# Kernel tuning notes

Measured on AMD Instinct MI355X. Metric: run time of the kernel, lower is better.

Reference implementation:

```python
import jax, jax.numpy as jnp
import numpy as np

N_NODES = 50000
N_EDGES = 800000
IN_DIM = 64
OUT_DIM = 64
HID = OUT_DIM // 2  # 32
N_LAYERS = 9  # layer_num; layer_num >= 7 => no temporal conv, conv dropout unused


def _layernorm(x, w, b, eps=1e-5):
    mu = jnp.mean(x, axis=-1, keepdims=True)
    var = jnp.var(x, axis=-1, keepdims=True)
    return (x - mu) * jax.lax.rsqrt(var + eps) * w + b


def _conv(x, Wp, Wn, Ws, src, tgt, pos_m, neg_m):
    # relation-wise gather -> linear -> masked merge -> single scatter_add
    xs = x[src]  # [E, d_in]
    m = jnp.where(pos_m[:, None], xs @ Wp.T, 0.0) + jnp.where(neg_m[:, None], xs @ Wn.T, 0.0)
    agg = jax.ops.segment_sum(m, tgt, num_segments=N_NODES)
    return agg + x @ Ws.T


def _asfr(x, ln_w, ln_b, gw, gb):
    xn = _layernorm(x, ln_w, ln_b)
    w = jax.nn.sigmoid(xn @ gw.T + gb)
    w1 = jnp.where(w > 0.5, 1.0, w)
    w2 = jnp.where(w > 0.5, 0.0, w)
    x1 = w1 * x
    x2 = w2 * x
    h = x.shape[1] // 2
    return jnp.concatenate([x1[:, :h] + x2[:, h:], x1[:, h:] + x2[:, :h]], axis=1)


def setup_inputs() -> dict:
    key = jax.random.key(0)
    ks = jax.random.split(key, 24)
    init_emb = jax.random.normal(ks[0], (N_NODES, IN_DIM), dtype=jnp.float32)
    src = jax.random.randint(ks[1], (N_EDGES,), 0, N_NODES)
    tgt = jax.random.randint(ks[2], (N_EDGES,), 0, N_NODES)
    sign = jnp.where(jax.random.uniform(ks[3], (N_EDGES,)) > 0.5, 1, -1).astype(jnp.int64)
    edge_index_s = jnp.stack([src, tgt, sign], axis=1).astype(jnp.int64)

    def w(k, shape, fan_in):
        return jax.random.normal(k, shape, dtype=jnp.float32) * (1.0 / np.sqrt(fan_in))

    inp = dict(init_emb=init_emb, edge_index_s=edge_index_s)
    # conv1: in 64 -> 32, relations pos/neg + self loop (no bias)
    inp["W1_pos"] = w(ks[4], (HID, IN_DIM), IN_DIM)
    inp["W1_neg"] = w(ks[5], (HID, IN_DIM), IN_DIM)
    inp["W1_self"] = w(ks[6], (HID, IN_DIM), IN_DIM)
    # 8 further convs: 32 -> 32, stacked
    L = N_LAYERS - 1
    inp["Wl_pos"] = w(ks[7], (L, HID, HID), HID)
    inp["Wl_neg"] = w(ks[8], (L, HID, HID), HID)
    inp["Wl_self"] = w(ks[9], (L, HID, HID), HID)
    # ASFR
    inp["asfr_ln_w"] = jnp.ones((HID,), jnp.float32)
    inp["asfr_ln_b"] = jnp.zeros((HID,), jnp.float32)
    inp["asfr_gate_w"] = w(ks[10], (HID, HID), HID)
    inp["asfr_gate_b"] = jnp.zeros((HID,), jnp.float32)
    # projection 32 -> 64
    inp["proj_w"] = w(ks[11], (OUT_DIM, HID), HID)
    inp["proj_b"] = jnp.zeros((OUT_DIM,), jnp.float32)
    # readout MLP: 64 -> 64 -> 64 -> 1, layernorm + relu between
    inp["mlp_w1"] = w(ks[12], (OUT_DIM, OUT_DIM), OUT_DIM)
    inp["mlp_b1"] = jnp.zeros((OUT_DIM,), jnp.float32)
    inp["mlp_ln1_w"] = jnp.ones((OUT_DIM,), jnp.float32)
    inp["mlp_ln1_b"] = jnp.zeros((OUT_DIM,), jnp.float32)
    inp["mlp_w2"] = w(ks[13], (OUT_DIM, OUT_DIM), OUT_DIM)
    inp["mlp_b2"] = jnp.zeros((OUT_DIM,), jnp.float32)
    inp["mlp_ln2_w"] = jnp.ones((OUT_DIM,), jnp.float32)
    inp["mlp_ln2_b"] = jnp.zeros((OUT_DIM,), jnp.float32)
    inp["mlp_w3"] = w(ks[14], (1, OUT_DIM), OUT_DIM)
    inp["mlp_b3"] = jnp.zeros((1,), jnp.float32)
    return inp


def reference(init_emb, edge_index_s, W1_pos, W1_neg, W1_self, Wl_pos, Wl_neg, Wl_self,
              asfr_ln_w, asfr_ln_b, asfr_gate_w, asfr_gate_b, proj_w, proj_b,
              mlp_w1, mlp_b1, mlp_ln1_w, mlp_ln1_b, mlp_w2, mlp_b2,
              mlp_ln2_w, mlp_ln2_b, mlp_w3, mlp_b3):
    src = edge_index_s[:, 0]
    tgt = edge_index_s[:, 1]
    sign = edge_index_s[:, 2]
    pos_m = sign > 0
    neg_m = sign < 0

    z = jax.nn.elu(_conv(init_emb, W1_pos, W1_neg, W1_self, src, tgt, pos_m, neg_m))
    z = _asfr(z, asfr_ln_w, asfr_ln_b, asfr_gate_w, asfr_gate_b)
    for i in range(Wl_pos.shape[0]):
        z_new = jax.nn.elu(_conv(z, Wl_pos[i], Wl_neg[i], Wl_self[i], src, tgt, pos_m, neg_m))
        z = z_new if i == 0 else z_new + 0.1 * z
    z = jax.nn.elu(z @ proj_w.T + proj_b)
    # readout MLP (eval mode: dropout identity)
    h = jax.nn.relu(_layernorm(z @ mlp_w1.T + mlp_b1, mlp_ln1_w, mlp_ln1_b))
    h = jax.nn.relu(_layernorm(h @ mlp_w2.T + mlp_b2, mlp_ln2_w, mlp_ln2_b))
    prob = jax.nn.sigmoid(h @ mlp_w3.T + mlp_b3)
    return (z, prob)
```

## Files before the change

kernel.cpp:

```cpp
#include <hip/hip_runtime.h>
#include <hip/hip_bf16.h>

#define NODES 50000
#define EDGES 800000
#define BSH 8
#define NBUCK 196
#define NBIN_BLOCKS 391

__device__ __forceinline__ float elu1(float x) { return x > 0.f ? x : expm1f(x); }

union F4 { float4 v; float f[4]; };

__global__ __launch_bounds__(256) void k_hist2(const int* __restrict__ ei, int* __restrict__ deg,
                                               int* __restrict__ bucket_cnt) {
  __shared__ int cnt[NBUCK];
  int t = threadIdx.x;
  for (int i = t; i < NBUCK; i += 256) cnt[i] = 0;
  __syncthreads();
  int base = blockIdx.x * 2048;
#pragma unroll
  for (int i = 0; i < 8; i++) {
    int e = base + i * 256 + t;
    if (e < EDGES) {
      int tgt = ei[e * 3 + 1];
      atomicAdd(deg + tgt, 1);
      atomicAdd(&cnt[tgt >> BSH], 1);
    }
  }
  __syncthreads();
  for (int i = t; i < NBUCK; i += 256)
    if (cnt[i]) atomicAdd(bucket_cnt + i, cnt[i]);
}

__global__ __launch_bounds__(512) void k_scan1(const int* __restrict__ deg, int* __restrict__ offs,
                                               int* __restrict__ bsum) {
  __shared__ int s[512];
  int t = threadIdx.x, i = blockIdx.x * 512 + t;
  int v = (i < NODES) ? deg[i] : 0;
  s[t] = v;
  __syncthreads();
  for (int o = 1; o < 512; o <<= 1) {
    int x = (t >= o) ? s[t - o] : 0;
    __syncthreads();
    s[t] += x;
    __syncthreads();
  }
  if (i < NODES) offs[i] = s[t] - v;
  if (t == 511) bsum[blockIdx.x] = s[511];
}

__global__ __launch_bounds__(128) void k_scan2(int* __restrict__ bsum, int nb) {
  __shared__ int s[128];
  int t = threadIdx.x;
  int v = (t < nb) ? bsum[t] : 0;
  s[t] = v;
  __syncthreads();
  for (int o = 1; o < 128; o <<= 1) {
    int x = (t >= o) ? s[t - o] : 0;
    __syncthreads();
    s[t] += x;
    __syncthreads();
  }
  if (t < nb) bsum[t] = s[t] - v;
}

__global__ __launch_bounds__(512) void k_scan3(int* __restrict__ offs, const int* __restrict__ bsum) {
  int i = blockIdx.x * 512 + threadIdx.x;
  if (i < NODES) offs[i] += bsum[blockIdx.x];
  if (i == 0) offs[NODES] = EDGES;
}

__global__ __launch_bounds__(256) void k_bscan(const int* __restrict__ bucket_cnt,
                                               int* __restrict__ bucket_base,
                                               int* __restrict__ bucket_cursor) {
  __shared__ int s[256];
  int t = threadIdx.x;
  int v = (t < NBUCK) ? bucket_cnt[t] : 0;
  s[t] = v;
  __syncthreads();
  for (int o = 1; o < 256; o <<= 1) {
    int x = (t >= o) ? s[t - o] : 0;
    __syncthreads();
    s[t] += x;
    __syncthreads();
  }
  if (t < NBUCK) { int e = s[t] - v; bucket_base[t] = e; bucket_cursor[t] = e; }
}

__global__ __launch_bounds__(256) void k_bin(const int* __restrict__ ei,
                                             int* __restrict__ bucket_cursor,
                                             uint2* __restrict__ binned) {
  __shared__ int cnt[NBUCK], base[NBUCK];
  int t = threadIdx.x;
  for (int i = t; i < NBUCK; i += 256) cnt[i] = 0;
  __syncthreads();
  int eb = blockIdx.x * 2048;
#pragma unroll
  for (int i = 0; i < 8; i++) {
    int e = eb + i * 256 + t;
    if (e < EDGES) atomicAdd(&cnt[ei[e * 3 + 1] >> BSH], 1);
  }
  __syncthreads();
  for (int i = t; i < NBUCK; i += 256) {
    int c = cnt[i];
    base[i] = c ? atomicAdd(bucket_cursor + i, c) : 0;
    cnt[i] = 0;
  }
  __syncthreads();
#pragma unroll
  for (int i = 0; i < 8; i++) {
    int e = eb + i * 256 + t;
    if (e < EDGES) {
      int src = ei[e * 3 + 0];
      int tgt = ei[e * 3 + 1];
      int sg  = ei[e * 3 + 2];
      unsigned val = (unsigned)src | (sg < 0 ? 0x80000000u : 0u);
      int bkt = tgt >> BSH;
      int r = atomicAdd(&cnt[bkt], 1);
      binned[base[bkt] + r] = make_uint2(val, (unsigned)tgt);
    }
  }
}

__global__ __launch_bounds__(256) void k_scatter2(const uint2* __restrict__ binned,
                                                  const int* __restrict__ bucket_base,
                                                  const int* __restrict__ bucket_cnt,
                                                  const int* __restrict__ offs,
                                                  unsigned* __restrict__ perm) {
  __shared__ int cur[256];
  int b = blockIdx.x, t = threadIdx.x;
  int t0 = b << BSH;
  cur[t] = (t0 + t < NODES) ? offs[t0 + t] : 0;
  __syncthreads();
  int n = bucket_cnt[b], bb = bucket_base[b];
  for (int i = t; i < n; i += 256) {
    uint2 e = binned[bb + i];
    int p = atomicAdd(&cur[e.y - t0], 1);
    perm[p] = e.x;
  }
}

__global__ __launch_bounds__(256) void k_lin64(const float* __restrict__ x,
    const float* __restrict__ Wp, const float* __restrict__ Wn, const float* __restrict__ Ws,
    __hip_bfloat16* __restrict__ ypb, __hip_bfloat16* __restrict__ ynb, float* __restrict__ ys) {
  constexpr int K4 = 16;
  __shared__ float4 wp[K4][32], wn[K4][32], wsm[K4][32];
  __shared__ float4 xs[8][K4];
  for (int i = threadIdx.x; i < 32 * K4; i += 256) {
    int k4 = i >> 5, c = i & 31;
    wp[k4][c]  = ((const float4*)Wp)[c * K4 + k4];
    wn[k4][c]  = ((const float4*)Wn)[c * K4 + k4];
    wsm[k4][c] = ((const float4*)Ws)[c * K4 + k4];
  }
  int base = blockIdx.x * 8;
  for (int i = threadIdx.x; i < 8 * K4; i += 256) {
    int r = i / K4, k4 = i - r * K4;
    xs[r][k4] = ((const float4*)(x + (size_t)(base + r) * 64))[k4];
  }
  __syncthreads();
  int lane = threadIdx.x & 31, local = threadIdx.x >> 5;
  float ap = 0.f, an = 0.f, asf = 0.f;
#pragma unroll
  for (int k4 = 0; k4 < K4; k4++) {
    float4 xv = xs[local][k4];
    float4 a = wp[k4][lane], b = wn[k4][lane], c = wsm[k4][lane];
    ap  = fmaf(xv.w, a.w, fmaf(xv.z, a.z, fmaf(xv.y, a.y, fmaf(xv.x, a.x, ap))));
    an  = fmaf(xv.w, b.w, fmaf(xv.z, b.z, fmaf(xv.y, b.y, fmaf(xv.x, b.x, an))));
    asf = fmaf(xv.w, c.w, fmaf(xv.z, c.z, fmaf(xv.y, c.y, fmaf(xv.x, c.x, asf))));
  }
  size_t o = (size_t)(base + local) * 32 + lane;
  ypb[o] = __float2bfloat16(ap);
  ynb[o] = __float2bfloat16(an);
  ys[o] = asf;
}

#define ACC8(A, V)                                   \
  A[0] += __uint_as_float((V).x << 16);              \
  A[1] += __uint_as_float((V).x & 0xffff0000u);      \
  A[2] += __uint_as_float((V).y << 16);              \
  A[3] += __uint_as_float((V).y & 0xffff0000u);      \
  A[4] += __uint_as_float((V).z << 16);              \
  A[5] += __uint_as_float((V).z & 0xffff0000u);      \
  A[6] += __uint_as_float((V).w << 16);              \
  A[7] += __uint_as_float((V).w & 0xffff0000u);

template <int DO_ASFR, int DO_RES, int DO_LIN, int WRITE_Z>
__global__ __launch_bounds__(256) void k_layer(
    const unsigned short* __restrict__ ypi, const unsigned short* __restrict__ yni,
    float* __restrict__ ys,
    const unsigned* __restrict__ perm, const int* __restrict__ offs,
    float* __restrict__ z,
    const float* __restrict__ lnw, const float* __restrict__ lnb,
    const float* __restrict__ gw, const float* __restrict__ gb,
    const float* __restrict__ Wp, const float* __restrict__ Wn, const float* __restrict__ Ws,
    __hip_bfloat16* __restrict__ ypo, __hip_bfloat16* __restrict__ yno) {
  __shared__ float4 wps[8][32], wns[8][32], wss[8][32], gws[8][32];
  __shared__ float zrow[8][36], xrow[8][36];
  int t = threadIdx.x;
  if (DO_LIN) {
    int k4 = t >> 5, c = t & 31;
    wps[k4][c] = ((const float4*)Wp)[c * 8 + k4];
    wns[k4][c] = ((const float4*)Wn)[c * 8 + k4];
    wss[k4][c] = ((const float4*)Ws)[c * 8 + k4];
    if (DO_ASFR) gws[k4][c] = ((const float4*)gw)[c * 8 + k4];
  }
  int lane = t & 31, local = t >> 5;
  int node = blockIdx.x * 8 + local;
  int es = lane >> 2, fs = lane & 3;
  int beg = offs[node], end = offs[node + 1];
  float a0[8], a1[8], a2[8], a3[8];
#pragma unroll
  for (int i = 0; i < 8; i++) { a0[i] = 0.f; a1[i] = 0.f; a2[i] = 0.f; a3[i] = 0.f; }
  for (int base = beg; base < end; base += 32) {
    unsigned pe = (base + lane < end) ? perm[base + lane] : 0u;
    int rem = end - base;
    unsigned u0 = __shfl(pe, es, 32);
    unsigned u1 = __shfl(pe, es + 8, 32);
    const unsigned short* p0 = (u0 >> 31) ? yni : ypi;
    const unsigned short* p1 = (u1 >> 31) ? yni : ypi;
    uint4 v0 = *((const uint4*)(p0 + (size_t)(u0 & 0x7FFFFFFFu) * 32) + fs);
    uint4 v1 = *((const uint4*)(p1 + (size_t)(u1 & 0x7FFFFFFFu) * 32) + fs);
    if (es < rem) { ACC8(a0, v0); }
    if (es + 8 < rem) { ACC8(a1, v1); }
    if (rem > 16) {
      unsigned u2 = __shfl(pe, es + 16, 32);
      unsigned u3 = __shfl(pe, es + 24, 32);
      const unsigned short* p2 = (u2 >> 31) ? yni : ypi;
      const unsigned short* p3 = (u3 >> 31) ? yni : ypi;
      uint4 v2 = *((const uint4*)(p2 + (size_t)(u2 & 0x7FFFFFFFu) * 32) + fs);
      uint4 v3 = *((const uint4*)(p3 + (size_t)(u3 & 0x7FFFFFFFu) * 32) + fs);
      if (es + 16 < rem) { ACC8(a2, v2); }
      if (es + 24 < rem) { ACC8(a3, v3); }
    }
  }
#pragma unroll
  for (int i = 0; i < 8; i++) a0[i] += (a1[i] + a2[i]) + a3[i];
#pragma unroll
  for (int m = 4; m <= 16; m <<= 1) {
#pragma unroll
    for (int i = 0; i < 8; i++) a0[i] += __shfl_xor(a0[i], m, 32);
  }
  if (es == 0) {
    const float* ysr = ys + (size_t)node * 32 + fs * 8;
    F4 s0, s1;
    s0.v = *(const float4*)ysr;
    s1.v = *(const float4*)(ysr + 4);
    float o[8];
#pragma unroll
    for (int i = 0; i < 4; i++) o[i] = elu1(a0[i] + s0.f[i]);
#pragma unroll
    for (int i = 0; i < 4; i++) o[4 + i] = elu1(a0[4 + i] + s1.f[i]);
    if (DO_RES) {
      const float* rr = z + (size_t)node * 32 + fs * 8;
      F4 r0, r1;
      r0.v = *(const float4*)rr;
      r1.v = *(const float4*)(rr + 4);
#pragma unroll
      for (int i = 0; i < 4; i++) { o[i] += 0.1f * r0.f[i]; o[4 + i] += 0.1f * r1.f[i]; }
    }
#pragma unroll
    for (int i = 0; i < 8; i++) zrow[local][fs * 8 + i] = o[i];
    if (WRITE_Z) {
      float* zw = z + (size_t)node * 32 + fs * 8;
      *(float4*)zw = make_float4(o[0], o[1], o[2], o[3]);
      *(float4*)(zw + 4) = make_float4(o[4], o[5], o[6], o[7]);
    }
  }
  __syncthreads();
  if (!DO_LIN) return;
  if (DO_ASFR) {
    float v = zrow[local][lane];
    float s = v;
#pragma unroll
    for (int m = 16; m; m >>= 1) s += __shfl_xor(s, m, 32);
    float mu = s * (1.f / 32.f);
    float d = v - mu, sq = d * d;
#pragma unroll
    for (int m = 16; m; m >>= 1) sq += __shfl_xor(sq, m, 32);
    float xn = d * rsqrtf(sq * (1.f / 32.f) + 1e-5f) * lnw[lane] + lnb[lane];
    xrow[local][lane] = xn;
    float ga = gb[lane];
#pragma unroll
    for (int k4 = 0; k4 < 8; k4++) {
      float4 xv = *((const float4*)&xrow[local][0] + k4);
      float4 w = gws[k4][lane];
      ga = fmaf(xv.w, w.w, fmaf(xv.z, w.z, fmaf(xv.y, w.y, fmaf(xv.x, w.x, ga))));
    }
    float g = 1.f / (1.f + __expf(-ga));
    float w1 = g > 0.5f ? 1.f : g;
    float w2 = g > 0.5f ? 0.f : g;
    float zn = w1 * v + __shfl_xor(w2 * v, 16, 32);
    zrow[local][lane] = zn;
  }
  float ap = 0.f, an = 0.f, asf = 0.f;
#pragma unroll
  for (int k4 = 0; k4 < 8; k4++) {
    float4 xv = *((const float4*)&zrow[local][0] + k4);
    float4 a2w = wps[k4][lane], b2 = wns[k4][lane], c2 = wss[k4][lane];
    ap  = fmaf(xv.w, a2w.w, fmaf(xv.z, a2w.z, fmaf(xv.y, a2w.y, fmaf(xv.x, a2w.x, ap))));
    an  = fmaf(xv.w, b2.w, fmaf(xv.z, b2.z, fmaf(xv.y, b2.y, fmaf(xv.x, b2.x, an))));
    asf = fmaf(xv.w, c2.w, fmaf(xv.z, c2.z, fmaf(xv.y, c2.y, fmaf(xv.x, c2.x, asf))));
  }
  size_t o = (size_t)node * 32 + lane;
  ypo[o] = __float2bfloat16(ap);
  yno[o] = __float2bfloat16(an);
  ys[o] = asf;
}

__global__ __launch_bounds__(256) void k_mlp(const float* __restrict__ z,
    const float* __restrict__ pw, const float* __restrict__ pb,
    const float* __restrict__ w1, const float* __restrict__ b1,
    const float* __restrict__ l1w, const float* __restrict__ l1b,
    const float* __restrict__ w2, const float* __restrict__ b2,
    const float* __restrict__ l2w, const float* __restrict__ l2b,
    const float* __restrict__ w3, const float* __restrict__ b3,
    float* __restrict__ outz, float* __restrict__ outp) {
  __shared__ float4 wbuf[1536];
  __shared__ float4 hbuf4[32 * 17];
  __shared__ float pb_s[64], b1_s[64], l1w_s[64], l1b_s[64], b2_s[64], l2w_s[64], l2b_s[64], w3_s[64];
  int t = threadIdx.x;
  for (int i = t; i < 512; i += 256) {
    int k = i >> 4, j4 = i & 15;
    float4 v;
    v.x = pw[(j4 * 4 + 0) * 32 + k]; v.y = pw[(j4 * 4 + 1) * 32 + k];
    v.z = pw[(j4 * 4 + 2) * 32 + k]; v.w = pw[(j4 * 4 + 3) * 32 + k];
    wbuf[i] = v;
  }
  for (int i = t; i < 1024; i += 256) {
    int k = i >> 4, j4 = i & 15;
    float4 v;
    v.x = w1[(j4 * 4 + 0) * 64 + k]; v.y = w1[(j4 * 4 + 1) * 64 + k];
    v.z = w1[(j4 * 4 + 2) * 64 + k]; v.w = w1[(j4 * 4 + 3) * 64 + k];
    wbuf[512 + i] = v;
  }
  if (t < 64) {
    pb_s[t] = pb[t]; b1_s[t] = b1[t]; l1w_s[t] = l1w[t]; l1b_s[t] = l1b[t];
    b2_s[t] = b2[t]; l2w_s[t] = l2w[t]; l2b_s[t] = l2b[t]; w3_s[t] = w3[t];
  }
  __syncthreads();
  int g = t >> 3, q = t & 7;
  int node = blockIdx.x * 32 + g;
  bool live = node < NODES;
  float bb3 = b3[0];
  float acc[8], h[8];
  if (live) {
    hbuf4[g * 17 + q] = ((const float4*)(z + (size_t)node * 32))[q];
#pragma unroll
    for (int i = 0; i < 8; i++) acc[i] = pb_s[q * 8 + i];
#pragma unroll 2
    for (int k4 = 0; k4 < 8; k4++) {
      F4 hv; hv.v = hbuf4[g * 17 + k4];
#pragma unroll
      for (int c = 0; c < 4; c++) {
        float hk = hv.f[c];
        float4 wa = wbuf[(k4 * 4 + c) * 16 + q * 2];
        float4 wb = wbuf[(k4 * 4 + c) * 16 + q * 2 + 1];
        acc[0] = fmaf(hk, wa.x, acc[0]); acc[1] = fmaf(hk, wa.y, acc[1]);
        acc[2] = fmaf(hk, wa.z, acc[2]); acc[3] = fmaf(hk, wa.w, acc[3]);
        acc[4] = fmaf(hk, wb.x, acc[4]); acc[5] = fmaf(hk, wb.y, acc[5]);
        acc[6] = fmaf(hk, wb.z, acc[6]); acc[7] = fmaf(hk, wb.w, acc[7]);
      }
    }
#pragma unroll
    for (int i = 0; i < 8; i++) h[i] = elu1(acc[i]);
    float4 h0 = make_float4(h[0], h[1], h[2], h[3]);
    float4 h1 = make_float4(h[4], h[5], h[6], h[7]);
    float4* oz = (float4*)(outz + (size_t)node * 64 + q * 8);
    oz[0] = h0; oz[1] = h1;
    hbuf4[g * 17 + 2 * q] = h0;
    hbuf4[g * 17 + 2 * q + 1] = h1;
#pragma unroll
    for (int i = 0; i < 8; i++) acc[i] = b1_s[q * 8 + i];
#pragma unroll 2
    for (int k4 = 0; k4 < 16; k4++) {
      F4 hv; hv.v = hbuf4[g * 17 + k4];
#pragma unroll
      for (int c = 0; c < 4; c++) {
        float hk = hv.f[c];
        float4 wa = wbuf[512 + (k4 * 4 + c) * 16 + q * 2];
        float4 wb = wbuf[512 + (k4 * 4 + c) * 16 + q * 2 + 1];
        acc[0] = fmaf(hk, wa.x, acc[0]); acc[1] = fmaf(hk, wa.y, acc[1]);
        acc[2] = fmaf(hk, wa.z, acc[2]); acc[3] = fmaf(hk, wa.w, acc[3]);
        acc[4] = fmaf(hk, wb.x, acc[4]); acc[5] = fmaf(hk, wb.y, acc[5]);
        acc[6] = fmaf(hk, wb.z, acc[6]); acc[7] = fmaf(hk, wb.w, acc[7]);
      }
    }
  }
  __syncthreads();
  for (int i = t; i < 1024; i += 256) {
    int k = i >> 4, j4 = i & 15;
    float4 v;
    v.x = w2[(j4 * 4 + 0) * 64 + k]; v.y = w2[(j4 * 4 + 1) * 64 + k];
    v.z = w2[(j4 * 4 + 2) * 64 + k]; v.w = w2[(j4 * 4 + 3) * 64 + k];
    wbuf[i] = v;
  }
  if (live) {
    float s = 0.f;
#pragma unroll
    for (int i = 0; i < 8; i++) s += acc[i];
    s += __shfl_xor(s, 1, 8); s += __shfl_xor(s, 2, 8); s += __shfl_xor(s, 4, 8);
    float mu = s * (1.f / 64.f);
    float vs = 0.f;
#pragma unroll
    for (int i = 0; i < 8; i++) { float dd = acc[i] - mu; vs += dd * dd; }
    vs += __shfl_xor(vs, 1, 8); vs += __shfl_xor(vs, 2, 8); vs += __shfl_xor(vs, 4, 8);
    float rs = rsqrtf(vs * (1.f / 64.f) + 1e-5f);
#pragma unroll
    for (int i = 0; i < 8; i++)
      h[i] = fmaxf((acc[i] - mu) * rs * l1w_s[q * 8 + i] + l1b_s[q * 8 + i], 0.f);
  }
  __syncthreads();
  if (!live) return;
  hbuf4[g * 17 + 2 * q] = make_float4(h[0], h[1], h[2], h[3]);
  hbuf4[g * 17 + 2 * q + 1] = make_float4(h[4], h[5], h[6], h[7]);
#pragma unroll
  for (int i = 0; i < 8; i++) acc[i] = b2_s[q * 8 + i];
#pragma unroll 2
  for (int k4 = 0; k4 < 16; k4++) {
    F4 hv; hv.v = hbuf4[g * 17 + k4];
#pragma unroll
    for (int c = 0; c < 4; c++) {
      float hk = hv.f[c];
      float4 wa = wbuf[(k4 * 4 + c) * 16 + q * 2];
      float4 wb = wbuf[(k4 * 4 + c) * 16 + q * 2 + 1];
      acc[0] = fmaf(hk, wa.x, acc[0]); acc[1] = fmaf(hk, wa.y, acc[1]);
      acc[2] = fmaf(hk, wa.z, acc[2]); acc[3] = fmaf(hk, wa.w, acc[3]);
      acc[4] = fmaf(hk, wb.x, acc[4]); acc[5] = fmaf(hk, wb.y, acc[5]);
      acc[6] = fmaf(hk, wb.z, acc[6]); acc[7] = fmaf(hk, wb.w, acc[7]);
    }
  }
  {
    float s = 0.f;
#pragma unroll
    for (int i = 0; i < 8; i++) s += acc[i];
    s += __shfl_xor(s, 1, 8); s += __shfl_xor(s, 2, 8); s += __shfl_xor(s, 4, 8);
    float mu = s * (1.f / 64.f);
    float vs = 0.f;
#pragma unroll
    for (int i = 0; i < 8; i++) { float dd = acc[i] - mu; vs += dd * dd; }
    vs += __shfl_xor(vs, 1, 8); vs += __shfl_xor(vs, 2, 8); vs += __shfl_xor(vs, 4, 8);
    float rs = rsqrtf(vs * (1.f / 64.f) + 1e-5f);
    float p = 0.f;
#pragma unroll
    for (int i = 0; i < 8; i++) {
      float hv2 = fmaxf((acc[i] - mu) * rs * l2w_s[q * 8 + i] + l2b_s[q * 8 + i], 0.f);
      p = fmaf(hv2, w3_s[q * 8 + i], p);
    }
    p += __shfl_xor(p, 1, 8); p += __shfl_xor(p, 2, 8); p += __shfl_xor(p, 4, 8);
    if (q == 0) outp[node] = 1.f / (1.f + __expf(-(p + bb3)));
  }
}

extern "C" void kernel_launch(void* const* d_in, const int* in_sizes, int n_in,
                              void* d_out, int out_size, void* d_ws, size_t ws_size,
                              hipStream_t stream) {
  const float* init_emb = (const float*)d_in[0];
  const int*   ei  = (const int*)d_in[1];
  const float* W1p = (const float*)d_in[2];
  const float* W1n = (const float*)d_in[3];
  const float* W1s = (const float*)d_in[4];
  const float* Wlp = (const float*)d_in[5];
  const float* Wln = (const float*)d_in[6];
  const float* Wls = (const float*)d_in[7];
  const float* lnw = (const float*)d_in[8];
  const float* lnb = (const float*)d_in[9];
  const float* gw  = (const float*)d_in[10];
  const float* gb  = (const float*)d_in[11];
  const float* pw  = (const float*)d_in[12];
  const float* pb  = (const float*)d_in[13];
  const float* w1  = (const float*)d_in[14];
  const float* b1  = (const float*)d_in[15];
  const float* l1w = (const float*)d_in[16];
  const float* l1b = (const float*)d_in[17];
  const float* w2  = (const float*)d_in[18];
  const float* b2  = (const float*)d_in[19];
  const float* l2w = (const float*)d_in[20];
  const float* l2b = (const float*)d_in[21];
  const float* w3  = (const float*)d_in[22];
  const float* b3  = (const float*)d_in[23];

  char* ws = (char*)d_ws;
  size_t off = 0;
  auto alloc = [&](size_t b) { void* p = ws + off; off = (off + b + 255) & ~(size_t)255; return p; };
  __hip_bfloat16* ypA = (__hip_bfloat16*)alloc(NODES * 32 * 2);
  __hip_bfloat16* ynA = (__hip_bfloat16*)alloc(NODES * 32 * 2);
  __hip_bfloat16* ypB = (__hip_bfloat16*)alloc(NODES * 32 * 2);
  __hip_bfloat16* ynB = (__hip_bfloat16*)alloc(NODES * 32 * 2);
  float*    ysel   = (float*)alloc(NODES * 32 * 4);
  float*    zbuf   = (float*)alloc(NODES * 32 * 4);
  unsigned* perm   = (unsigned*)alloc(EDGES * 4);
  int*      deg    = (int*)alloc(NODES * 4);
  int*      offs   = (int*)alloc((NODES + 1) * 4);
  int*      bsum   = (int*)alloc(128 * 4);
  int*      bucket_cnt    = (int*)alloc(NBUCK * 4);
  int*      bucket_base   = (int*)alloc(NBUCK * 4);
  int*      bucket_cursor = (int*)alloc(NBUCK * 4);
  uint2*    binned = (uint2*)ypA;

  hipMemsetAsync(deg, 0, NODES * 4, stream);
  hipMemsetAsync(bucket_cnt, 0, NBUCK * 4, stream);
  k_hist2<<<NBIN_BLOCKS, 256, 0, stream>>>(ei, deg, bucket_cnt);
  int nb = (NODES + 511) / 512;
  k_scan1<<<nb, 512, 0, stream>>>(deg, offs, bsum);
  k_scan2<<<1, 128, 0, stream>>>(bsum, nb);
  k_scan3<<<nb, 512, 0, stream>>>(offs, bsum);
  k_bscan<<<1, 256, 0, stream>>>(bucket_cnt, bucket_base, bucket_cursor);
  k_bin<<<NBIN_BLOCKS, 256, 0, stream>>>(ei, bucket_cursor, binned);
  k_scatter2<<<NBUCK, 256, 0, stream>>>(binned, bucket_base, bucket_cnt, offs, perm);

  const int G = NODES / 8;
  k_lin64<<<G, 256, 0, stream>>>(init_emb, W1p, W1n, W1s, ypA, ynA, ysel);
  k_layer<1, 0, 1, 0><<<G, 256, 0, stream>>>((const unsigned short*)ypA, (const unsigned short*)ynA,
      ysel, perm, offs, zbuf, lnw, lnb, gw, gb, Wlp, Wln, Wls, ypB, ynB);
  k_layer<0, 0, 1, 1><<<G, 256, 0, stream>>>((const unsigned short*)ypB, (const unsigned short*)ynB,
      ysel, perm, offs, zbuf, nullptr, nullptr, nullptr, nullptr,
      Wlp + 1024, Wln + 1024, Wls + 1024, ypA, ynA);
  const __hip_bfloat16* yin_p = ypA; const __hip_bfloat16* yin_n = ynA;
  __hip_bfloat16* yout_p = ypB; __hip_bfloat16* yout_n = ynB;
  for (int i = 1; i < 7; i++) {
    k_layer<0, 1, 1, 1><<<G, 256, 0, stream>>>((const unsigned short*)yin_p, (const unsigned short*)yin_n,
        ysel, perm, offs, zbuf, nullptr, nullptr, nullptr, nullptr,
        Wlp + (i + 1) * 1024, Wln + (i + 1) * 1024, Wls + (i + 1) * 1024, yout_p, yout_n);
    const __hip_bfloat16* tp = yin_p; const __hip_bfloat16* tn = yin_n;
    yin_p = yout_p; yin_n = yout_n;
    yout_p = (__hip_bfloat16*)tp; yout_n = (__hip_bfloat16*)tn;
  }
  k_layer<0, 1, 0, 1><<<G, 256, 0, stream>>>((const unsigned short*)yin_p, (const unsigned short*)yin_n,
      ysel, perm, offs, zbuf, nullptr, nullptr, nullptr, nullptr,
      nullptr, nullptr, nullptr, nullptr, nullptr);

  float* outz = (float*)d_out;
  float* outp = outz + (size_t)NODES * 64;
  k_mlp<<<(NODES + 31) / 32, 256, 0, stream>>>(zbuf, pw, pb, w1, b1, l1w, l1b,
                                               w2, b2, l2w, l2b, w3, b3, outz, outp);
}
```

Before: 395.0 us.

## Pack binned edges into 32-bit words and process four nodes per MLP thread group

The binning pass now packs the source index, the sign bit and the target's low 8 bits into one 32-bit word instead of a uint2, halving the binned edge traffic. The scatter pass unpacks it and rebuilds the original sign-in-top-bit format. The readout MLP kernel now handles 128 nodes per block, four per 8-lane group, so each shared-memory weight load is reused across four nodes. The price is more registers per thread and fewer blocks, and the packing assumes node ids fit in 16 bits (NODES is 50000, so they do).

```diff
diff --git a/kernel.cpp b/kernel.cpp
--- a/kernel.cpp
+++ b/kernel.cpp
@@ -89,7 +89,7 @@
 
 __global__ __launch_bounds__(256) void k_bin(const int* __restrict__ ei,
                                              int* __restrict__ bucket_cursor,
-                                             uint2* __restrict__ binned) {
+                                             unsigned* __restrict__ binned) {
   __shared__ int cnt[NBUCK], base[NBUCK];
   int t = threadIdx.x;
   for (int i = t; i < NBUCK; i += 256) cnt[i] = 0;
@@ -114,15 +114,15 @@
       int src = ei[e * 3 + 0];
       int tgt = ei[e * 3 + 1];
       int sg  = ei[e * 3 + 2];
-      unsigned val = (unsigned)src | (sg < 0 ? 0x80000000u : 0u);
+      unsigned val = (unsigned)src | (sg < 0 ? 0x10000u : 0u) | ((unsigned)(tgt & 255) << 17);
       int bkt = tgt >> BSH;
       int r = atomicAdd(&cnt[bkt], 1);
-      binned[base[bkt] + r] = make_uint2(val, (unsigned)tgt);
-    }
-  }
-}
-
-__global__ __launch_bounds__(256) void k_scatter2(const uint2* __restrict__ binned,
+      binned[base[bkt] + r] = val;
+    }
+  }
+}
+
+__global__ __launch_bounds__(256) void k_scatter2(const unsigned* __restrict__ binned,
                                                   const int* __restrict__ bucket_base,
                                                   const int* __restrict__ bucket_cnt,
                                                   const int* __restrict__ offs,
@@ -134,9 +134,9 @@
   __syncthreads();
   int n = bucket_cnt[b], bb = bucket_base[b];
   for (int i = t; i < n; i += 256) {
-    uint2 e = binned[bb + i];
-    int p = atomicAdd(&cur[e.y - t0], 1);
-    perm[p] = e.x;
+    unsigned e = binned[bb + i];
+    int p = atomicAdd(&cur[(e >> 17) & 255], 1);
+    perm[p] = (e & 0xFFFFu) | ((e & 0x10000u) << 15);
   }
 }
 
@@ -316,7 +316,7 @@
     const float* __restrict__ w3, const float* __restrict__ b3,
     float* __restrict__ outz, float* __restrict__ outp) {
   __shared__ float4 wbuf[1536];
-  __shared__ float4 hbuf4[32 * 17];
+  __shared__ float4 hbuf4[128 * 17];
   __shared__ float pb_s[64], b1_s[64], l1w_s[64], l1b_s[64], b2_s[64], l2w_s[64], l2b_s[64], w3_s[64];
   int t = threadIdx.x;
   for (int i = t; i < 512; i += 256) {
@@ -339,50 +339,72 @@
   }
   __syncthreads();
   int g = t >> 3, q = t & 7;
-  int node = blockIdx.x * 32 + g;
-  bool live = node < NODES;
+  int nb0 = blockIdx.x * 128 + g;
   float bb3 = b3[0];
-  float acc[8], h[8];
-  if (live) {
-    hbuf4[g * 17 + q] = ((const float4*)(z + (size_t)node * 32))[q];
-#pragma unroll
-    for (int i = 0; i < 8; i++) acc[i] = pb_s[q * 8 + i];
+  bool live[4];
+#pragma unroll
+  for (int n = 0; n < 4; n++) live[n] = (nb0 + 32 * n) < NODES;
+  float acc[4][8], h[4][8];
+#pragma unroll
+  for (int n = 0; n < 4; n++)
+    if (live[n])
+      hbuf4[(n * 32 + g) * 17 + q] = ((const float4*)(z + (size_t)(nb0 + 32 * n) * 32))[q];
+#pragma unroll
+  for (int n = 0; n < 4; n++)
+#pragma unroll
+    for (int i = 0; i < 8; i++) acc[n][i] = pb_s[q * 8 + i];
 #pragma unroll 2
-    for (int k4 = 0; k4 < 8; k4++) {
-      F4 hv; hv.v = hbuf4[g * 17 + k4];
-#pragma unroll
-      for (int c = 0; c < 4; c++) {
-        float hk = hv.f[c];
-        float4 wa = wbuf[(k4 * 4 + c) * 16 + q * 2];
-        float4 wb = wbuf[(k4 * 4 + c) * 16 + q * 2 + 1];
-        acc[0] = fmaf(hk, wa.x, acc[0]); acc[1] = fmaf(hk, wa.y, acc[1]);
-        acc[2] = fmaf(hk, wa.z, acc[2]); acc[3] = fmaf(hk, wa.w, acc[3]);
-        acc[4] = fmaf(hk, wb.x, acc[4]); acc[5] = fmaf(hk, wb.y, acc[5]);
-        acc[6] = fmaf(hk, wb.z, acc[6]); acc[7] = fmaf(hk, wb.w, acc[7]);
+  for (int k4 = 0; k4 < 8; k4++) {
+    F4 hv[4];
+#pragma unroll
+    for (int n = 0; n < 4; n++) hv[n].v = hbuf4[(n * 32 + g) * 17 + k4];
+#pragma unroll
+    for (int c = 0; c < 4; c++) {
+      float4 wa = wbuf[(k4 * 4 + c) * 16 + q * 2];
+      float4 wb = wbuf[(k4 * 4 + c) * 16 + q * 2 + 1];
+#pragma unroll
+      for (int n = 0; n < 4; n++) {
+        float hk = hv[n].f[c];
+        acc[n][0] = fmaf(hk, wa.x, acc[n][0]); acc[n][1] = fmaf(hk, wa.y, acc[n][1]);
+        acc[n][2] = fmaf(hk, wa.z, acc[n][2]); acc[n][3] = fmaf(hk, wa.w, acc[n][3]);
+        acc[n][4] = fmaf(hk, wb.x, acc[n][4]); acc[n][5] = fmaf(hk, wb.y, acc[n][5]);
+        acc[n][6] = fmaf(hk, wb.z, acc[n][6]); acc[n][7] = fmaf(hk, wb.w, acc[n][7]);
       }
     }
-#pragma unroll
-    for (int i = 0; i < 8; i++) h[i] = elu1(acc[i]);
-    float4 h0 = make_float4(h[0], h[1], h[2], h[3]);
-    float4 h1 = make_float4(h[4], h[5], h[6], h[7]);
-    float4* oz = (float4*)(outz + (size_t)node * 64 + q * 8);
-    oz[0] = h0; oz[1] = h1;
-    hbuf4[g * 17 + 2 * q] = h0;
-    hbuf4[g * 17 + 2 * q + 1] = h1;
-#pragma unroll
-    for (int i = 0; i < 8; i++) acc[i] = b1_s[q * 8 + i];
+  }
+#pragma unroll
+  for (int n = 0; n < 4; n++) {
+#pragma unroll
+    for (int i = 0; i < 8; i++) h[n][i] = elu1(acc[n][i]);
+    float4 h0 = make_float4(h[n][0], h[n][1], h[n][2], h[n][3]);
+    float4 h1 = make_float4(h[n][4], h[n][5], h[n][6], h[n][7]);
+    if (live[n]) {
+      float4* oz = (float4*)(outz + (size_t)(nb0 + 32 * n) * 64 + q * 8);
+      oz[0] = h0; oz[1] = h1;
+    }
+    hbuf4[(n * 32 + g) * 17 + 2 * q] = h0;
+    hbuf4[(n * 32 + g) * 17 + 2 * q + 1] = h1;
+  }
+#pragma unroll
+  for (int n = 0; n < 4; n++)
+#pragma unroll
+    for (int i = 0; i < 8; i++) acc[n][i] = b1_s[q * 8 + i];
 #pragma unroll 2
-    for (int k4 = 0; k4 < 16; k4++) {
-      F4 hv; hv.v = hbuf4[g * 17 + k4];
-#pragma unroll
-      for (int c = 0; c < 4; c++) {
-        float hk = hv.f[c];
-        float4 wa = wbuf[512 + (k4 * 4 + c) * 16 + q * 2];
-        float4 wb = wbuf[512 + (k4 * 4 + c) * 16 + q * 2 + 1];
-        acc[0] = fmaf(hk, wa.x, acc[0]); acc[1] = fmaf(hk, wa.y, acc[1]);
-        acc[2] = fmaf(hk, wa.z, acc[2]); acc[3] = fmaf(hk, wa.w, acc[3]);
-        acc[4] = fmaf(hk, wb.x, acc[4]); acc[5] = fmaf(hk, wb.y, acc[5]);
-        acc[6] = fmaf(hk, wb.z, acc[6]); acc[7] = fmaf(hk, wb.w, acc[7]);
+  for (int k4 = 0; k4 < 16; k4++) {
+    F4 hv[4];
+#pragma unroll
+    for (int n = 0; n < 4; n++) hv[n].v = hbuf4[(n * 32 + g) * 17 + k4];
+#pragma unroll
+    for (int c = 0; c < 4; c++) {
+      float4 wa = wbuf[512 + (k4 * 4 + c) * 16 + q * 2];
+      float4 wb = wbuf[512 + (k4 * 4 + c) * 16 + q * 2 + 1];
+#pragma unroll
+      for (int n = 0; n < 4; n++) {
+        float hk = hv[n].f[c];
+        acc[n][0] = fmaf(hk, wa.x, acc[n][0]); acc[n][1] = fmaf(hk, wa.y, acc[n][1]);
+        acc[n][2] = fmaf(hk, wa.z, acc[n][2]); acc[n][3] = fmaf(hk, wa.w, acc[n][3]);
+        acc[n][4] = fmaf(hk, wb.x, acc[n][4]); acc[n][5] = fmaf(hk, wb.y, acc[n][5]);
+        acc[n][6] = fmaf(hk, wb.z, acc[n][6]); acc[n][7] = fmaf(hk, wb.w, acc[n][7]);
       }
     }
   }
@@ -394,60 +416,71 @@
     v.z = w2[(j4 * 4 + 2) * 64 + k]; v.w = w2[(j4 * 4 + 3) * 64 + k];
     wbuf[i] = v;
   }
-  if (live) {
+#pragma unroll
+  for (int n = 0; n < 4; n++) {
     float s = 0.f;
 #pragma unroll
-    for (int i = 0; i < 8; i++) s += acc[i];
+    for (int i = 0; i < 8; i++) s += acc[n][i];
     s += __shfl_xor(s, 1, 8); s += __shfl_xor(s, 2, 8); s += __shfl_xor(s, 4, 8);
     float mu = s * (1.f / 64.f);
     float vs = 0.f;
 #pragma unroll
-    for (int i = 0; i < 8; i++) { float dd = acc[i] - mu; vs += dd * dd; }
+    for (int i = 0; i < 8; i++) { float dd = acc[n][i] - mu; vs += dd * dd; }
     vs += __shfl_xor(vs, 1, 8); vs += __shfl_xor(vs, 2, 8); vs += __shfl_xor(vs, 4, 8);
     float rs = rsqrtf(vs * (1.f / 64.f) + 1e-5f);
 #pragma unroll
     for (int i = 0; i < 8; i++)
-      h[i] = fmaxf((acc[i] - mu) * rs * l1w_s[q * 8 + i] + l1b_s[q * 8 + i], 0.f);
-  }
-  __syncthreads();
-  if (!live) return;
-  hbuf4[g * 17 + 2 * q] = make_float4(h[0], h[1], h[2], h[3]);
-  hbuf4[g * 17 + 2 * q + 1] = make_float4(h[4], h[5], h[6], h[7]);
-#pragma unroll
-  for (int i = 0; i < 8; i++) acc[i] = b2_s[q * 8 + i];
+      h[n][i] = fmaxf((acc[n][i] - mu) * rs * l1w_s[q * 8 + i] + l1b_s[q * 8 + i], 0.f);
+  }
+  __syncthreads();
+#pragma unroll
+  for (int n = 0; n < 4; n++) {
+    hbuf4[(n * 32 + g) * 17 + 2 * q] = make_float4(h[n][0], h[n][1], h[n][2], h[n][3]);
+    hbuf4[(n * 32 + g) * 17 + 2 * q + 1] = make_float4(h[n][4], h[n][5], h[n][6], h[n][7]);
+  }
+#pragma unroll
+  for (int n = 0; n < 4; n++)
+#pragma unroll
+    for (int i = 0; i < 8; i++) acc[n][i] = b2_s[q * 8 + i];
 #pragma unroll 2
   for (int k4 = 0; k4 < 16; k4++) {
-    F4 hv; hv.v = hbuf4[g * 17 + k4];
+    F4 hv[4];
+#pragma unroll
+    for (int n = 0; n < 4; n++) hv[n].v = hbuf4[(n * 32 + g) * 17 + k4];
 #pragma unroll
     for (int c = 0; c < 4; c++) {
-      float hk = hv.f[c];
       float4 wa = wbuf[(k4 * 4 + c) * 16 + q * 2];
       float4 wb = wbuf[(k4 * 4 + c) * 16 + q * 2 + 1];
-      acc[0] = fmaf(hk, wa.x, acc[0]); acc[1] = fmaf(hk, wa.y, acc[1]);
-      acc[2] = fmaf(hk, wa.z, acc[2]); acc[3] = fmaf(hk, wa.w, acc[3]);
-      acc[4] = fmaf(hk, wb.x, acc[4]); acc[5] = fmaf(hk, wb.y, acc[5]);
-      acc[6] = fmaf(hk, wb.z, acc[6]); acc[7] = fmaf(hk, wb.w, acc[7]);
-    }
-  }
-  {
+#pragma unroll
+      for (int n = 0; n < 4; n++) {
+        float hk = hv[n].f[c];
+        acc[n][0] = fmaf(hk, wa.x, acc[n][0]); acc[n][1] = fmaf(hk, wa.y, acc[n][1]);
+        acc[n][2] = fmaf(hk, wa.z, acc[n][2]); acc[n][3] = fmaf(hk, wa.w, acc[n][3]);
+        acc[n][4] = fmaf(hk, wb.x, acc[n][4]); acc[n][5] = fmaf(hk, wb.y, acc[n][5]);
+        acc[n][6] = fmaf(hk, wb.z, acc[n][6]); acc[n][7] = fmaf(hk, wb.w, acc[n][7]);
+      }
+    }
+  }
+#pragma unroll
+  for (int n = 0; n < 4; n++) {
     float s = 0.f;
 #pragma unroll
-    for (int i = 0; i < 8; i++) s += acc[i];
+    for (int i = 0; i < 8; i++) s += acc[n][i];
     s += __shfl_xor(s, 1, 8); s += __shfl_xor(s, 2, 8); s += __shfl_xor(s, 4, 8);
     float mu = s * (1.f / 64.f);
     float vs = 0.f;
 #pragma unroll
-    for (int i = 0; i < 8; i++) { float dd = acc[i] - mu; vs += dd * dd; }
+    for (int i = 0; i < 8; i++) { float dd = acc[n][i] - mu; vs += dd * dd; }
     vs += __shfl_xor(vs, 1, 8); vs += __shfl_xor(vs, 2, 8); vs += __shfl_xor(vs, 4, 8);
     float rs = rsqrtf(vs * (1.f / 64.f) + 1e-5f);
     float p = 0.f;
 #pragma unroll
     for (int i = 0; i < 8; i++) {
-      float hv2 = fmaxf((acc[i] - mu) * rs * l2w_s[q * 8 + i] + l2b_s[q * 8 + i], 0.f);
+      float hv2 = fmaxf((acc[n][i] - mu) * rs * l2w_s[q * 8 + i] + l2b_s[q * 8 + i], 0.f);
       p = fmaf(hv2, w3_s[q * 8 + i], p);
     }
     p += __shfl_xor(p, 1, 8); p += __shfl_xor(p, 2, 8); p += __shfl_xor(p, 4, 8);
-    if (q == 0) outp[node] = 1.f / (1.f + __expf(-(p + bb3)));
+    if (q == 0 && live[n]) outp[nb0 + 32 * n] = 1.f / (1.f + __expf(-(p + bb3)));
   }
 }
 
@@ -495,7 +528,7 @@
   int*      bucket_cnt    = (int*)alloc(NBUCK * 4);
   int*      bucket_base   = (int*)alloc(NBUCK * 4);
   int*      bucket_cursor = (int*)alloc(NBUCK * 4);
-  uint2*    binned = (uint2*)ypA;
+  unsigned* binned = (unsigned*)ypA;
 
   hipMemsetAsync(deg, 0, NODES * 4, stream);
   hipMemsetAsync(bucket_cnt, 0, NBUCK * 4, stream);
@@ -531,6 +564,6 @@
 
   float* outz = (float*)d_out;
   float* outp = outz + (size_t)NODES * 64;
-  k_mlp<<<(NODES + 31) / 32, 256, 0, stream>>>(zbuf, pw, pb, w1, b1, l1w, l1b,
-                                               w2, b2, l2w, l2b, w3, b3, outz, outp);
-}
+  k_mlp<<<(NODES + 127) / 128, 256, 0, stream>>>(zbuf, pw, pb, w1, b1, l1w, l1b,
+                                                 w2, b2, l2w, l2b, w3, b3, outz, outp);
+}
```

Measured after the change: 381.0 us. -3.5%, faster.
